# Kernel tuning notes

Hardware: AMD Instinct MI355X
Metric: run time of the kernel (lower is better)

## Reference

```python
import jax, jax.numpy as jnp
import numpy as np

D_IN = 128
D_H = 128
N_CHILD = 8
BATCH = 32768


def setup_inputs() -> dict:
    key = jax.random.key(0)
    ks = jax.random.split(key, 16)
    stdev = 1.0 / np.sqrt(D_H)

    def unif(k, shape):
        return jax.random.uniform(k, shape, jnp.float32, -stdev, stdev)

    inp = {
        "x": jax.random.normal(ks[0], (BATCH, D_IN), jnp.float32),
        "h": jax.random.normal(ks[1], (N_CHILD, BATCH, D_H), jnp.float32),
        "C": jax.random.normal(ks[2], (N_CHILD, BATCH, D_H), jnp.float32),
        "W_i": unif(ks[3], (D_IN, D_H)),
        "W_f": unif(ks[4], (D_IN, D_H)),
        "W_o": unif(ks[5], (D_IN, D_H)),
        "W_u": unif(ks[6], (D_IN, D_H)),
        "U_i": unif(ks[7], (D_H, D_H)),
        "U_f": unif(ks[8], (D_H, D_H)),
        "U_o": unif(ks[9], (D_H, D_H)),
        "U_u": unif(ks[10], (D_H, D_H)),
        "b_i": unif(ks[11], (1, D_H)),
        "b_f": unif(ks[12], (1, D_H)),
        "b_o": unif(ks[13], (1, D_H)),
        "b_u": unif(ks[14], (1, D_H)),
    }
    return inp


def reference(x, h, C, W_i, W_f, W_o, W_u, U_i, U_f, U_o, U_u, b_i, b_f, b_o, b_u):
    # x: [B, D_in]; h, C: [N_child, B, H]
    h_tilde = jnp.sum(h, axis=0)  # [B, H]
    i_j = jax.nn.sigmoid(x @ W_i + h_tilde @ U_i + b_i)  # [B, H]
    o_j = jax.nn.sigmoid(x @ W_o + h_tilde @ U_o + b_o)  # [B, H]
    f_x = x @ W_f  # [B, H]
    # per-child forget gates, vectorized over the child axis
    f_j = jax.nn.sigmoid(f_x[None] + jnp.einsum('nbh,hk->nbk', h, U_f) + b_f)  # [N, B, H]
    u_j = jnp.tanh(x @ W_u + h_tilde @ U_u + b_u)  # [B, H]
    c_j = i_j * u_j + jnp.sum(f_j * C, axis=0)  # [B, H]
    h_j = o_j * jnp.tanh(c_j)
    return (h_j, c_j)
```

## Files before the change

### kernel.cpp

```cpp
#include <hip/hip_runtime.h>

#define NB 32768
#define NCH 8
#define ROWS 16

typedef __bf16 bf16x8 __attribute__((ext_vector_type(8)));
typedef float f32x4 __attribute__((ext_vector_type(4)));
typedef unsigned int u32;
typedef unsigned short u16;
typedef u32 u32x4v __attribute__((ext_vector_type(4)));
typedef u32 u32x2v __attribute__((ext_vector_type(2)));

__device__ __align__(16) u16 g_wt[8 * 128 * 128];

__device__ __forceinline__ u16 f2bf(float f) {
  u32 u = __builtin_bit_cast(u32, f);
  u32 r = u + 0x7FFFu + ((u >> 16) & 1u);
  return (u16)(r >> 16);
}
__device__ __forceinline__ float sigm(float s) {
  return __builtin_amdgcn_rcpf(1.0f + __expf(-s));
}
__device__ __forceinline__ float tanh_f(float v) {
  float e = __expf(2.0f * v);
  return 1.0f - 2.0f * __builtin_amdgcn_rcpf(e + 1.0f);
}

__global__ void prep_weights(const float* __restrict__ Wi, const float* __restrict__ Wf,
                             const float* __restrict__ Wo, const float* __restrict__ Wu,
                             const float* __restrict__ Ui, const float* __restrict__ Uf,
                             const float* __restrict__ Uo, const float* __restrict__ Uu) {
  __shared__ float t[128][129];
  const float* srcs[8] = {Wi, Wf, Wo, Wu, Ui, Uf, Uo, Uu};
  const float* s = srcs[blockIdx.x];
  for (int i = threadIdx.x; i < 16384; i += 256) t[i >> 7][i & 127] = s[i];
  __syncthreads();
  u16* dst = g_wt + blockIdx.x * 16384;
  for (int i = threadIdx.x; i < 16384; i += 256) {
    int n = i >> 7, k = i & 127;
    dst[i] = f2bf(t[k][n]);
  }
}

__device__ __forceinline__ bf16x8 ldA(const u32x4v* buf, int row, int ks, int g) {
  u32x4v v = buf[row * 16 + ((ks * 4 + g) ^ (row & 7))];
  return __builtin_bit_cast(bf16x8, v);
}
__device__ __forceinline__ bf16x8 ldB(const u16* wt, int col, int ks, int g) {
  return __builtin_bit_cast(bf16x8, *(const u32x4v*)(wt + col * 128 + ks * 32 + g * 8));
}

__device__ __forceinline__ void stage_load16(const float* __restrict__ src, int tid,
                                             f32x4 v[2]) {
#pragma unroll
  for (int i = 0; i < 2; ++i) {
    int q = tid + (i << 8);
    v[i] = *(const f32x4*)(src + (q >> 5) * 128 + (q & 31) * 4);
  }
}
__device__ __forceinline__ void stage_write16(u32x4v* buf, int tid, const f32x4 v[2]) {
  u32x2v* b2 = (u32x2v*)buf;
#pragma unroll
  for (int i = 0; i < 2; ++i) {
    int q = tid + (i << 8);
    int r = q >> 5, c4 = q & 31;
    u32x2v p;
    p[0] = (u32)f2bf(v[i][0]) | ((u32)f2bf(v[i][1]) << 16);
    p[1] = (u32)f2bf(v[i][2]) | ((u32)f2bf(v[i][3]) << 16);
    b2[r * 32 + (c4 ^ ((r & 7) << 1))] = p;
  }
}

__device__ __forceinline__ void stage_gll_swz(const float* __restrict__ src, float* dst,
                                              int lane, int wv) {
#pragma unroll
  for (int i = 0; i < 2; ++i) {
    int r0 = wv * 4 + i * 2;
    int row = r0 + (lane >> 5);
    const float* g = src + row * 128 + (((lane & 31) ^ (row & 7)) << 2);
    __builtin_amdgcn_global_load_lds(
        (const __attribute__((address_space(1))) void*)g,
        (__attribute__((address_space(3))) void*)(dst + r0 * 128), 16, 0, 0);
  }
}
__device__ __forceinline__ void stage_gll_csw(const float* __restrict__ src, float* dst,
                                              int lane, int wv) {
#pragma unroll
  for (int i = 0; i < 2; ++i) {
    int r0 = wv * 4 + i * 2;
    int row = r0 + (lane >> 5);
    const float* g = src + row * 128 + (((lane & 31) ^ (((row >> 2) & 3) << 2)) << 2);
    __builtin_amdgcn_global_load_lds(
        (const __attribute__((address_space(1))) void*)g,
        (__attribute__((address_space(3))) void*)(dst + r0 * 128), 16, 0, 0);
  }
}
__device__ __forceinline__ bf16x8 ldAf(const float* buf, int row, int ks, int g) {
  int s = row & 7;
  const float* base = buf + row * 128 + ks * 32;
  f32x4 lo = *(const f32x4*)(base + (((g * 2) ^ s) << 2));
  f32x4 hi = *(const f32x4*)(base + (((g * 2 + 1) ^ s) << 2));
  bf16x8 r;
  r[0] = (__bf16)lo[0]; r[1] = (__bf16)lo[1]; r[2] = (__bf16)lo[2]; r[3] = (__bf16)lo[3];
  r[4] = (__bf16)hi[0]; r[5] = (__bf16)hi[1]; r[6] = (__bf16)hi[2]; r[7] = (__bf16)hi[3];
  return r;
}

__device__ __forceinline__ void gemm_g16(const u32x4v* a, const u16* wt, int cl, int g,
                                         int cb, f32x4 acc[2]) {
#pragma unroll
  for (int ks = 0; ks < 4; ++ks) {
    bf16x8 b0 = ldB(wt, cb + cl, ks, g);
    bf16x8 b1 = ldB(wt, cb + 16 + cl, ks, g);
    bf16x8 a0 = ldA(a, cl, ks, g);
    acc[0] = __builtin_amdgcn_mfma_f32_16x16x32_bf16(a0, b0, acc[0], 0, 0, 0);
    acc[1] = __builtin_amdgcn_mfma_f32_16x16x32_bf16(a0, b1, acc[1], 0, 0, 0);
  }
}

__device__ __forceinline__ int fxsw(int row, int dw) {
  int k = (row >> 2) & 3;
  return row * 128 + (dw ^ (((k & 1) << 4) | ((k >> 1) << 2)));
}
__device__ __forceinline__ void exch16(float* ex, const f32x4 fr[2], int g, int cl,
                                       int cb, int tid, f32x4 s4[2]) {
  __syncthreads();
#pragma unroll
  for (int nf = 0; nf < 2; ++nf) {
    int col = cb + nf * 16 + cl;
#pragma unroll
    for (int r_ = 0; r_ < 4; ++r_)
      ex[fxsw(g * 4 + r_, col)] = fr[nf][r_];
  }
  __syncthreads();
  int sr = tid >> 5, sc = (tid & 31) * 4;
#pragma unroll
  for (int i = 0; i < 2; ++i)
    s4[i] = *(const f32x4*)(ex + fxsw(sr + i * 8, sc));
}

__global__ __launch_bounds__(256, 4) void tree_lstm(
    const float* __restrict__ x, const float* __restrict__ h, const float* __restrict__ C,
    const float* __restrict__ b_i, const float* __restrict__ b_f,
    const float* __restrict__ b_o, const float* __restrict__ b_u,
    float* __restrict__ out) {
  __shared__ float hbf[2][ROWS * 128];
  __shared__ float cbf[2][ROWS * 128];
  __shared__ u32x4v xs[ROWS * 16];

  const int tid = threadIdx.x;
  const int lane = tid & 63;
  const int wv = tid >> 6;
  const int cb = wv * 32;
  const int row0 = blockIdx.x * ROWS;
  const int g = lane >> 4;
  const int cl = lane & 15;
  const int sr = tid >> 5;
  const int sc = (tid & 31) * 4;
  const f32x4 fz = {0.f, 0.f, 0.f, 0.f};

  stage_gll_swz(h + (size_t)row0 * 128, hbf[0], lane, wv);
  stage_gll_csw(C + (size_t)row0 * 128, cbf[0], lane, wv);
  f32x4 xv[2];
  stage_load16(x + (size_t)row0 * 128, tid, xv);

  const float bf0 = b_f[cb + cl], bf1 = b_f[cb + 16 + cl];
  const float bi0 = b_i[cb + cl], bi1 = b_i[cb + 16 + cl];
  const float bo0 = b_o[cb + cl], bo1 = b_o[cb + 16 + cl];
  const float bu0 = b_u[cb + cl], bu1 = b_u[cb + 16 + cl];

  stage_write16(xs, tid, xv);
  __syncthreads();

  bf16x8 uf0[4], uf1[4];
#pragma unroll
  for (int ks = 0; ks < 4; ++ks) {
    uf0[ks] = ldB(g_wt + 5 * 16384, cb + cl, ks, g);
    uf1[ks] = ldB(g_wt + 5 * 16384, cb + 16 + cl, ks, g);
  }

  f32x4 afx[2] = {fz, fz};
  gemm_g16(xs, g_wt + 1 * 16384, cl, g, cb, afx);

  f32x4 accc[2] = {fz, fz};
  f32x4 htacc[2] = {fz, fz};

  for (int n = 0; n < NCH; ++n) {
    if (n + 1 < NCH) {
      stage_gll_swz(h + ((size_t)(n + 1) * NB + row0) * 128, hbf[(n + 1) & 1], lane, wv);
      stage_gll_csw(C + ((size_t)(n + 1) * NB + row0) * 128, cbf[(n + 1) & 1], lane, wv);
    }
    __builtin_amdgcn_sched_barrier(0);

    const float* hcur = hbf[n & 1];
    f32x4 f[2] = {afx[0], afx[1]};
#pragma unroll
    for (int ks = 0; ks < 4; ++ks) {
      bf16x8 a0 = ldAf(hcur, cl, ks, g);
      f[0] = __builtin_amdgcn_mfma_f32_16x16x32_bf16(a0, uf0[ks], f[0], 0, 0, 0);
      f[1] = __builtin_amdgcn_mfma_f32_16x16x32_bf16(a0, uf1[ks], f[1], 0, 0, 0);
    }

#pragma unroll
    for (int i = 0; i < 2; ++i) {
      int q = tid + (i << 8);
      int r = q >> 5, c4 = q & 31;
      htacc[i] += *(const f32x4*)(hcur + r * 128 + ((c4 ^ (r & 7)) << 2));
    }

    const float* ccur = cbf[n & 1];
#pragma unroll
    for (int nf = 0; nf < 2; ++nf) {
      float bfv = nf ? bf1 : bf0;
      int lc = (cb + nf * 16 + cl) ^ (g << 4);
#pragma unroll
      for (int r = 0; r < 4; ++r)
        accc[nf][r] += sigm(f[nf][r] + bfv) * ccur[(g * 4 + r) * 128 + lc];
    }
    __syncthreads();
  }

  stage_write16((u32x4v*)hbf[0], tid, htacc);
  __syncthreads();
  const u32x4v* ht = (const u32x4v*)hbf[0];
  float* ex = cbf[0];

  f32x4 pre[2], s4[2];

  pre[0] = fz; pre[1] = fz;
  gemm_g16(xs, g_wt + 3 * 16384, cl, g, cb, pre);
  gemm_g16(ht, g_wt + 7 * 16384, cl, g, cb, pre);
  f32x4 uF[2];
#pragma unroll
  for (int nf = 0; nf < 2; ++nf) {
    float bv = nf ? bu1 : bu0;
#pragma unroll
    for (int r = 0; r < 4; ++r) uF[nf][r] = tanh_f(pre[nf][r] + bv);
  }

  pre[0] = fz; pre[1] = fz;
  gemm_g16(xs, g_wt + 0 * 16384, cl, g, cb, pre);
  gemm_g16(ht, g_wt + 4 * 16384, cl, g, cb, pre);
  f32x4 cF[2], tF[2];
#pragma unroll
  for (int nf = 0; nf < 2; ++nf) {
    float bv = nf ? bi1 : bi0;
#pragma unroll
    for (int r = 0; r < 4; ++r) {
      float cv = sigm(pre[nf][r] + bv) * uF[nf][r] + accc[nf][r];
      cF[nf][r] = cv;
      tF[nf][r] = tanh_f(cv);
    }
  }
  exch16(ex, cF, g, cl, cb, tid, s4);
  float* outc = out + (size_t)NB * 128;
#pragma unroll
  for (int i = 0; i < 2; ++i)
    *(f32x4*)(outc + (size_t)(row0 + sr + i * 8) * 128 + sc) = s4[i];

  pre[0] = fz; pre[1] = fz;
  gemm_g16(xs, g_wt + 2 * 16384, cl, g, cb, pre);
  gemm_g16(ht, g_wt + 6 * 16384, cl, g, cb, pre);
  f32x4 hF[2];
#pragma unroll
  for (int nf = 0; nf < 2; ++nf) {
    float bv = nf ? bo1 : bo0;
#pragma unroll
    for (int r = 0; r < 4; ++r)
      hF[nf][r] = sigm(pre[nf][r] + bv) * tF[nf][r];
  }
  exch16(ex, hF, g, cl, cb, tid, s4);
#pragma unroll
  for (int i = 0; i < 2; ++i)
    *(f32x4*)(out + (size_t)(row0 + sr + i * 8) * 128 + sc) = s4[i];
}

extern "C" void kernel_launch(void* const* d_in, const int* in_sizes, int n_in,
                              void* d_out, int out_size, void* d_ws, size_t ws_size,
                              hipStream_t stream) {
  (void)in_sizes; (void)n_in; (void)out_size; (void)d_ws; (void)ws_size;
  const float* x = (const float*)d_in[0];
  const float* h = (const float*)d_in[1];
  const float* C = (const float*)d_in[2];

  prep_weights<<<8, 256, 0, stream>>>(
      (const float*)d_in[3], (const float*)d_in[4], (const float*)d_in[5],
      (const float*)d_in[6], (const float*)d_in[7], (const float*)d_in[8],
      (const float*)d_in[9], (const float*)d_in[10]);

  tree_lstm<<<NB / ROWS, 256, 0, stream>>>(
      x, h, C,
      (const float*)d_in[11], (const float*)d_in[12],
      (const float*)d_in[13], (const float*)d_in[14],
      (float*)d_out);
}
```

Measured before the change: 131.9 us.

## Triple-buffer child h/C staging with explicit vmcnt waits and fully unrolled loop

New measurement: 180.1 us. +36.6%, slower.

```diff
diff --git a/kernel.cpp b/kernel.cpp
--- a/kernel.cpp
+++ b/kernel.cpp
@@ -3,6 +3,12 @@
 #define NB 32768
 #define NCH 8
 #define ROWS 16
+
+#define WAITV8 asm volatile("s_waitcnt vmcnt(8)" ::: "memory")
+#define WAITV4 asm volatile("s_waitcnt vmcnt(4)" ::: "memory")
+#define WAITV0 asm volatile("s_waitcnt vmcnt(0)" ::: "memory")
+#define WAITL0 asm volatile("s_waitcnt lgkmcnt(0)" ::: "memory")
+#define MEMFENCE asm volatile("" ::: "memory")
 
 typedef __bf16 bf16x8 __attribute__((ext_vector_type(8)));
 typedef float f32x4 __attribute__((ext_vector_type(4)));
@@ -139,13 +145,13 @@
     s4[i] = *(const f32x4*)(ex + fxsw(sr + i * 8, sc));
 }
 
-__global__ __launch_bounds__(256, 4) void tree_lstm(
+__global__ __launch_bounds__(256) void tree_lstm(
     const float* __restrict__ x, const float* __restrict__ h, const float* __restrict__ C,
     const float* __restrict__ b_i, const float* __restrict__ b_f,
     const float* __restrict__ b_o, const float* __restrict__ b_u,
     float* __restrict__ out) {
-  __shared__ float hbf[2][ROWS * 128];
-  __shared__ float cbf[2][ROWS * 128];
+  __shared__ float hbf[3][ROWS * 128];
+  __shared__ float cbf[3][ROWS * 128];
   __shared__ u32x4v xs[ROWS * 16];
 
   const int tid = threadIdx.x;
@@ -159,11 +165,8 @@
   const int sc = (tid & 31) * 4;
   const f32x4 fz = {0.f, 0.f, 0.f, 0.f};
 
-  stage_gll_swz(h + (size_t)row0 * 128, hbf[0], lane, wv);
-  stage_gll_csw(C + (size_t)row0 * 128, cbf[0], lane, wv);
   f32x4 xv[2];
   stage_load16(x + (size_t)row0 * 128, tid, xv);
-
   const float bf0 = b_f[cb + cl], bf1 = b_f[cb + 16 + cl];
   const float bi0 = b_i[cb + cl], bi1 = b_i[cb + 16 + cl];
   const float bo0 = b_o[cb + cl], bo1 = b_o[cb + 16 + cl];
@@ -178,21 +181,27 @@
     uf0[ks] = ldB(g_wt + 5 * 16384, cb + cl, ks, g);
     uf1[ks] = ldB(g_wt + 5 * 16384, cb + 16 + cl, ks, g);
   }
-
   f32x4 afx[2] = {fz, fz};
   gemm_g16(xs, g_wt + 1 * 16384, cl, g, cb, afx);
+  __builtin_amdgcn_sched_barrier(0);
+
+#pragma unroll
+  for (int k = 0; k < 3; ++k) {
+    stage_gll_swz(h + ((size_t)k * NB + row0) * 128, hbf[k], lane, wv);
+    stage_gll_csw(C + ((size_t)k * NB + row0) * 128, cbf[k], lane, wv);
+  }
+  __builtin_amdgcn_sched_barrier(0);
 
   f32x4 accc[2] = {fz, fz};
   f32x4 htacc[2] = {fz, fz};
 
+#pragma unroll
   for (int n = 0; n < NCH; ++n) {
-    if (n + 1 < NCH) {
-      stage_gll_swz(h + ((size_t)(n + 1) * NB + row0) * 128, hbf[(n + 1) & 1], lane, wv);
-      stage_gll_csw(C + ((size_t)(n + 1) * NB + row0) * 128, cbf[(n + 1) & 1], lane, wv);
-    }
-    __builtin_amdgcn_sched_barrier(0);
-
-    const float* hcur = hbf[n & 1];
+    if (n <= 5) { WAITV8; } else if (n == 6) { WAITV4; } else { WAITV0; }
+    __builtin_amdgcn_s_barrier();
+    MEMFENCE;
+
+    const float* hcur = hbf[n % 3];
     f32x4 f[2] = {afx[0], afx[1]};
 #pragma unroll
     for (int ks = 0; ks < 4; ++ks) {
@@ -208,7 +217,7 @@
       htacc[i] += *(const f32x4*)(hcur + r * 128 + ((c4 ^ (r & 7)) << 2));
     }
 
-    const float* ccur = cbf[n & 1];
+    const float* ccur = cbf[n % 3];
 #pragma unroll
     for (int nf = 0; nf < 2; ++nf) {
       float bfv = nf ? bf1 : bf0;
@@ -217,7 +226,14 @@
       for (int r = 0; r < 4; ++r)
         accc[nf][r] += sigm(f[nf][r] + bfv) * ccur[(g * 4 + r) * 128 + lc];
     }
-    __syncthreads();
+
+    WAITL0;
+    __builtin_amdgcn_s_barrier();
+    MEMFENCE;
+    if (n + 3 < NCH) {
+      stage_gll_swz(h + ((size_t)(n + 3) * NB + row0) * 128, hbf[n % 3], lane, wv);
+      stage_gll_csw(C + ((size_t)(n + 3) * NB + row0) * 128, cbf[n % 3], lane, wv);
+    }
   }
 
   stage_write16((u32x4v*)hbf[0], tid, htacc);
```
